# Kernel tuning notes

Hardware: AMD Instinct MI355X
Metric: run time of the kernel (lower is better)

The kernel has to match this reference:

```python
import jax, jax.numpy as jnp
import numpy as np

N, M, B, L, D = 100000, 256, 8, 128, 64
COORD_MAX = 1024


def setup_inputs() -> dict:
    key = jax.random.key(0)
    ks = jax.random.split(key, 9)
    # batch ids sorted so the original loop's centroid_offset == column index
    clu_b = jnp.sort(jax.random.randint(ks[0], (N, 1), 0, B))
    cen_b = jnp.sort(jax.random.randint(ks[1], (M, 1), 0, B))
    clu_xyz = jax.random.randint(ks[2], (N, 3), 0, COORD_MAX)
    cen_xyz = jax.random.randint(ks[3], (M, 3), 0, COORD_MAX)
    return {
        "cluster_coords": jnp.concatenate([clu_b, clu_xyz], axis=1).astype(jnp.int32),
        "centroid_coords": jnp.concatenate([cen_b, cen_xyz], axis=1).astype(jnp.int32),
        "cluster_feats": jax.random.normal(ks[4], (N, L), jnp.float32),
        "centroid_feats": jax.random.normal(ks[5], (M, L), jnp.float32),
        "centroid_conf": jax.random.uniform(ks[6], (M, 1), jnp.float32),
        "W": jax.random.normal(ks[7], (L, D), jnp.float32) * 0.05,
        "b": jax.random.normal(ks[8], (D,), jnp.float32) * 0.05,
    }


def reference(cluster_coords, centroid_coords, cluster_feats, centroid_feats,
              centroid_conf, W, b):
    # pointwise Conv3d(k=1) == linear on features
    clu = cluster_feats @ W + b                      # [N, D]
    nrm = jnp.maximum(jnp.linalg.norm(clu, axis=1, keepdims=True), 1e-12)
    clu = clu / nrm                                  # F.normalize(p=2, dim=1)
    cen = centroid_conf * (centroid_feats @ W + b)   # [M, D]

    # same-batch mask replaces the python loop + scatter
    valid = cluster_coords[:, 0][:, None] == centroid_coords[:, 0][None, :]  # [N, M]

    # pairwise L2 distance on spatial coords via squared expansion (exact for small ints)
    cc = cluster_coords[:, 1:].astype(jnp.float32)   # [N, 3]
    ec = centroid_coords[:, 1:].astype(jnp.float32)  # [M, 3]
    d2 = (jnp.sum(cc * cc, axis=1)[:, None]
          + jnp.sum(ec * ec, axis=1)[None, :]
          - 2.0 * cc @ ec.T)
    dist = jnp.maximum(jnp.sqrt(jnp.maximum(d2, 0.0)), 0.1)  # clamp(min=0.1)

    logits = jnp.where(valid, -dist, -jnp.inf)
    attn = jax.nn.softmax(logits, axis=-1)           # per-row over same-batch centroids
    attn = jnp.where(valid, attn, 0.0)               # rows w/ no centroids -> 0 (matches zeros init)

    out = (clu @ cen.T) * attn                       # [N, M]
    return out
```

## Files before the change

kernel.cpp:

```cpp
#include <hip/hip_runtime.h>
#include <stdint.h>


#define NN 100000
#define MM 256
#define BB 8
#define LL 128
#define DD 64
#define NTILES (NN / 16)

typedef float f32x4 __attribute__((ext_vector_type(4)));
typedef __bf16 bf16x8 __attribute__((ext_vector_type(8)));

union U16x8 { uint4 u; bf16x8 v; unsigned short s[8]; };

static __device__ __forceinline__ unsigned short f2bf(float f) {
  union { float f; unsigned int i; } t; t.f = f;
  unsigned int x = t.i;
  x += 0x7fffu + ((x >> 16) & 1u);
  return (unsigned short)(x >> 16);
}

__global__ __launch_bounds__(256) void prep_kernel(
    const int* __restrict__ cen_coords,
    const float* __restrict__ cen_feats,
    const float* __restrict__ conf,
    const float* __restrict__ W,
    const float* __restrict__ bvec,
    unsigned short* __restrict__ cen_ws,
    unsigned short* __restrict__ wt_ws,
    float4* __restrict__ cmeta_ws)
{
  int tid = threadIdx.x;
  if (blockIdx.x < 16) {
    int m = blockIdx.x * 16 + (tid >> 4);
    int c = tid & 15;
    float a0 = 0.f, a1 = 0.f, a2 = 0.f, a3 = 0.f;
    for (int l = 0; l < LL; l++) {
      float f = cen_feats[m * LL + l];
      const float* wr = W + l * DD + c;
      a0 += f * wr[0];  a1 += f * wr[16];
      a2 += f * wr[32]; a3 += f * wr[48];
    }
    float cf = conf[m];
    cen_ws[m * DD + c +  0] = f2bf(cf * (a0 + bvec[c +  0]));
    cen_ws[m * DD + c + 16] = f2bf(cf * (a1 + bvec[c + 16]));
    cen_ws[m * DD + c + 32] = f2bf(cf * (a2 + bvec[c + 32]));
    cen_ws[m * DD + c + 48] = f2bf(cf * (a3 + bvec[c + 48]));
  } else {
    for (int i = tid; i < LL * DD; i += 256) {
      int l = i >> 6, d = i & 63;
      wt_ws[d * LL + l] = f2bf(W[l * DD + d]);
    }
    {
      int4 cc = ((const int4*)cen_coords)[tid];
      float4 f; f.x = (float)cc.x; f.y = (float)cc.y; f.z = (float)cc.z; f.w = (float)cc.w;
      cmeta_ws[tid] = f;
    }
  }
}

__global__ __launch_bounds__(256) void main_kernel(
    const int* __restrict__ clu_coords,
    const float* __restrict__ feats,
    const float* __restrict__ bvec,
    const unsigned short* __restrict__ cen_ws,
    const unsigned short* __restrict__ wt_ws,
    const float4* __restrict__ cmeta_ws,
    float* __restrict__ out)
{
  __shared__ float4 cmeta_s[MM];
  __shared__ __align__(16) unsigned short clu_s[4][16 * 72];
  __shared__ int4 rmeta_s[4][16];
  __shared__ float2 rsoft_s[4][16];

  int tid = threadIdx.x;
  int wave = tid >> 6, lane = tid & 63;
  for (int i = tid; i < MM; i += 256) cmeta_s[i] = cmeta_ws[i];
  int tile = blockIdx.x * 4 + wave;
  bool live = tile < NTILES;
  if (live && lane < 16) rmeta_s[wave][lane] = ((const int4*)clu_coords)[tile * 16 + lane];
  __syncthreads();

  int q = lane >> 4, c = lane & 15;
  float inv_nrm[4];
  if (live) {
    f32x4 acc[4] = {{0,0,0,0},{0,0,0,0},{0,0,0,0},{0,0,0,0}};
    const float4* fb = (const float4*)(feats + (size_t)(tile * 16 + c) * LL);
    const uint4* wb = (const uint4*)wt_ws;
#pragma unroll
    for (int ks = 0; ks < 4; ks++) {
      float4 f0 = fb[ks * 8 + q * 2];
      float4 f1 = fb[ks * 8 + q * 2 + 1];
      U16x8 a;
      a.s[0] = f2bf(f0.x); a.s[1] = f2bf(f0.y); a.s[2] = f2bf(f0.z); a.s[3] = f2bf(f0.w);
      a.s[4] = f2bf(f1.x); a.s[5] = f2bf(f1.y); a.s[6] = f2bf(f1.z); a.s[7] = f2bf(f1.w);
#pragma unroll
      for (int nt = 0; nt < 4; nt++) {
        U16x8 b; b.u = wb[(nt * 16 + c) * 16 + ks * 4 + q];
        acc[nt] = __builtin_amdgcn_mfma_f32_16x16x32_bf16(a.v, b.v, acc[nt], 0, 0, 0);
      }
    }
#pragma unroll
    for (int nt = 0; nt < 4; nt++) {
      float bv = bvec[nt * 16 + c];
      acc[nt][0] += bv; acc[nt][1] += bv; acc[nt][2] += bv; acc[nt][3] += bv;
    }
#pragma unroll
    for (int r = 0; r < 4; r++) {
      float s = acc[0][r]*acc[0][r] + acc[1][r]*acc[1][r] + acc[2][r]*acc[2][r] + acc[3][r]*acc[3][r];
      s += __shfl_xor(s, 1); s += __shfl_xor(s, 2); s += __shfl_xor(s, 4); s += __shfl_xor(s, 8);
      inv_nrm[r] = 1.0f / fmaxf(sqrtf(s), 1e-12f);
    }
#pragma unroll
    for (int nt = 0; nt < 4; nt++)
#pragma unroll
      for (int r = 0; r < 4; r++)
        clu_s[wave][(q * 4 + r) * 72 + nt * 16 + c] = f2bf(acc[nt][r]);

    {
      int rr = lane >> 2, ss = lane & 3;
      int4 rm = rmeta_s[wave][rr];
      float rbf = (float)rm.x;
      float x = (float)rm.y, y = (float)rm.z, z = (float)rm.w;
      float dmin = 3.4e38f;
      for (int m = ss; m < MM; m += 4) {
        float4 cm = cmeta_s[m];
        if (cm.x == rbf) {
          float dx = x - cm.y, dy = y - cm.z, dz = z - cm.w;
          float d = fmaxf(sqrtf(dx*dx + dy*dy + dz*dz), 0.1f);
          dmin = fminf(dmin, d);
        }
      }
      dmin = fminf(dmin, __shfl_xor(dmin, 1));
      dmin = fminf(dmin, __shfl_xor(dmin, 2));
      if (!(dmin < 3.0e38f)) dmin = 0.f;
      float ssum = 0.f;
      for (int m = ss; m < MM; m += 4) {
        float4 cm = cmeta_s[m];
        if (cm.x == rbf) {
          float dx = x - cm.y, dy = y - cm.z, dz = z - cm.w;
          float d = fmaxf(sqrtf(dx*dx + dy*dy + dz*dz), 0.1f);
          ssum += __expf(dmin - d);
        }
      }
      ssum += __shfl_xor(ssum, 1);
      ssum += __shfl_xor(ssum, 2);
      float invden = ssum > 0.f ? 1.f / ssum : 0.f;
      rsoft_s[wave][rr] = make_float2(dmin, invden);
    }
  }
  __syncthreads();
  if (!live) return;

  const uint4* cb = (const uint4*)(clu_s[wave]);
  U16x8 a0, a1;
  a0.u = cb[c * 9 + q];
  a1.u = cb[c * 9 + 4 + q];

  float rx[4], ry[4], rz[4], sdmin[4], sinv[4];
  int rb[4];
#pragma unroll
  for (int r = 0; r < 4; r++) {
    int4 rm = rmeta_s[wave][q * 4 + r];
    rb[r] = rm.x; rx[r] = (float)rm.y; ry[r] = (float)rm.z; rz[r] = (float)rm.w;
    float2 sp = rsoft_s[wave][q * 4 + r];
    sdmin[r] = sp.x; sinv[r] = sp.y;
  }

  const uint4* cenb = (const uint4*)cen_ws;
  size_t orow = (size_t)(tile * 16) * MM;
#pragma unroll
  for (int mt = 0; mt < 16; mt++) {
    U16x8 b0, b1;
    b0.u = cenb[(mt * 16 + c) * 8 + q];
    b1.u = cenb[(mt * 16 + c) * 8 + 4 + q];
    f32x4 dacc = {0, 0, 0, 0};
    dacc = __builtin_amdgcn_mfma_f32_16x16x32_bf16(a0.v, b0.v, dacc, 0, 0, 0);
    dacc = __builtin_amdgcn_mfma_f32_16x16x32_bf16(a1.v, b1.v, dacc, 0, 0, 0);
    int m = mt * 16 + c;
    float4 cm = cmeta_s[m];
    int cbatch = (int)cm.x;
#pragma unroll
    for (int r = 0; r < 4; r++) {
      float dx = rx[r] - cm.y, dy = ry[r] - cm.z, dz = rz[r] - cm.w;
      float d = fmaxf(sqrtf(dx*dx + dy*dy + dz*dz), 0.1f);
      float w = __expf(fminf(sdmin[r] - d, 0.f)) * sinv[r] * inv_nrm[r];
      float val = (cbatch == rb[r]) ? dacc[r] * w : 0.f;
      out[orow + (size_t)(q * 4 + r) * MM + m] = val;
    }
  }
}

extern "C" void kernel_launch(void* const* d_in, const int* in_sizes, int n_in,
                              void* d_out, int out_size, void* d_ws, size_t ws_size,
                              hipStream_t stream) {
  const int* clu_coords = (const int*)d_in[0];
  const int* cen_coords = (const int*)d_in[1];
  const float* clu_feats = (const float*)d_in[2];
  const float* cen_feats = (const float*)d_in[3];
  const float* conf      = (const float*)d_in[4];
  const float* W         = (const float*)d_in[5];
  const float* bvec      = (const float*)d_in[6];
  float* out = (float*)d_out;

  char* ws = (char*)d_ws;
  unsigned short* cen_ws = (unsigned short*)ws;
  unsigned short* wt_ws  = (unsigned short*)(ws + 32768);
  float4* cmeta_ws       = (float4*)(ws + 32768 + 16384);

  prep_kernel<<<17, 256, 0, stream>>>(cen_coords, cen_feats, conf, W, bvec,
                                      cen_ws, wt_ws, cmeta_ws);
  main_kernel<<<(NTILES + 3) / 4, 256, 0, stream>>>(
      clu_coords, clu_feats, bvec, cen_ws, wt_ws, cmeta_ws, out);
}
```

Before: 226.5 us.

## Split each row tile across four waves with LDS-staged softmax and coalesced stores

Each block now handles one 16-row tile instead of four. Wave 0 does the feature projection while the other three waves compute partial min distances. All waves then compute the softmax weights into an LDS buffer and each wave does a quarter of the centroid MFMA columns. The output tile is written with coalesced float4 stores from LDS. This spreads the serial softmax loops across more threads and widens the stores, at the cost of more __syncthreads barriers, uncached global reads of the centroid metadata, and a larger LDS footprint per block.

Result: slower. 237.7 us (+5.0%).

```diff
diff --git a/kernel.cpp b/kernel.cpp
--- a/kernel.cpp
+++ b/kernel.cpp
@@ -4,10 +4,10 @@
 
 #define NN 100000
 #define MM 256
-#define BB 8
 #define LL 128
 #define DD 64
 #define NTILES (NN / 16)
+#define WP 260
 
 typedef float f32x4 __attribute__((ext_vector_type(4)));
 typedef __bf16 bf16x8 __attribute__((ext_vector_type(8)));
@@ -61,30 +61,27 @@
 }
 
 __global__ __launch_bounds__(256) void main_kernel(
-    const int* __restrict__ clu_coords,
+    const int4* __restrict__ clu_coords4,
     const float* __restrict__ feats,
     const float* __restrict__ bvec,
     const unsigned short* __restrict__ cen_ws,
     const unsigned short* __restrict__ wt_ws,
-    const float4* __restrict__ cmeta_ws,
+    const float4* __restrict__ cmeta,
     float* __restrict__ out)
 {
-  __shared__ float4 cmeta_s[MM];
-  __shared__ __align__(16) unsigned short clu_s[4][16 * 72];
-  __shared__ int4 rmeta_s[4][16];
-  __shared__ float2 rsoft_s[4][16];
+  __shared__ __align__(16) float w_s[16 * WP];
+  __shared__ __align__(16) unsigned short clu_s[16 * 72];
+  __shared__ float part_s[16][16];
+  __shared__ float dmin_s[16];
+  __shared__ float invn_s[16];
+  __shared__ float scale_s[16];
 
   int tid = threadIdx.x;
   int wave = tid >> 6, lane = tid & 63;
-  for (int i = tid; i < MM; i += 256) cmeta_s[i] = cmeta_ws[i];
-  int tile = blockIdx.x * 4 + wave;
-  bool live = tile < NTILES;
-  if (live && lane < 16) rmeta_s[wave][lane] = ((const int4*)clu_coords)[tile * 16 + lane];
-  __syncthreads();
-
+  int tile = blockIdx.x;
   int q = lane >> 4, c = lane & 15;
-  float inv_nrm[4];
-  if (live) {
+
+  if (wave == 0) {
     f32x4 acc[4] = {{0,0,0,0},{0,0,0,0},{0,0,0,0},{0,0,0,0}};
     const float4* fb = (const float4*)(feats + (size_t)(tile * 16 + c) * LL);
     const uint4* wb = (const uint4*)wt_ws;
@@ -110,84 +107,110 @@
     for (int r = 0; r < 4; r++) {
       float s = acc[0][r]*acc[0][r] + acc[1][r]*acc[1][r] + acc[2][r]*acc[2][r] + acc[3][r]*acc[3][r];
       s += __shfl_xor(s, 1); s += __shfl_xor(s, 2); s += __shfl_xor(s, 4); s += __shfl_xor(s, 8);
-      inv_nrm[r] = 1.0f / fmaxf(sqrtf(s), 1e-12f);
+      float invn = 1.0f / fmaxf(sqrtf(s), 1e-12f);
+      if (c == 0) invn_s[q * 4 + r] = invn;
     }
 #pragma unroll
     for (int nt = 0; nt < 4; nt++)
 #pragma unroll
       for (int r = 0; r < 4; r++)
-        clu_s[wave][(q * 4 + r) * 72 + nt * 16 + c] = f2bf(acc[nt][r]);
-
-    {
-      int rr = lane >> 2, ss = lane & 3;
-      int4 rm = rmeta_s[wave][rr];
-      float rbf = (float)rm.x;
-      float x = (float)rm.y, y = (float)rm.z, z = (float)rm.w;
-      float dmin = 3.4e38f;
-      for (int m = ss; m < MM; m += 4) {
-        float4 cm = cmeta_s[m];
-        if (cm.x == rbf) {
-          float dx = x - cm.y, dy = y - cm.z, dz = z - cm.w;
-          float d = fmaxf(sqrtf(dx*dx + dy*dy + dz*dz), 0.1f);
-          dmin = fminf(dmin, d);
-        }
-      }
-      dmin = fminf(dmin, __shfl_xor(dmin, 1));
-      dmin = fminf(dmin, __shfl_xor(dmin, 2));
-      if (!(dmin < 3.0e38f)) dmin = 0.f;
-      float ssum = 0.f;
-      for (int m = ss; m < MM; m += 4) {
-        float4 cm = cmeta_s[m];
-        if (cm.x == rbf) {
-          float dx = x - cm.y, dy = y - cm.z, dz = z - cm.w;
-          float d = fmaxf(sqrtf(dx*dx + dy*dy + dz*dz), 0.1f);
-          ssum += __expf(dmin - d);
-        }
-      }
-      ssum += __shfl_xor(ssum, 1);
-      ssum += __shfl_xor(ssum, 2);
-      float invden = ssum > 0.f ? 1.f / ssum : 0.f;
-      rsoft_s[wave][rr] = make_float2(dmin, invden);
-    }
-  }
-  __syncthreads();
-  if (!live) return;
-
-  const uint4* cb = (const uint4*)(clu_s[wave]);
-  U16x8 a0, a1;
-  a0.u = cb[c * 9 + q];
-  a1.u = cb[c * 9 + 4 + q];
-
-  float rx[4], ry[4], rz[4], sdmin[4], sinv[4];
-  int rb[4];
-#pragma unroll
-  for (int r = 0; r < 4; r++) {
-    int4 rm = rmeta_s[wave][q * 4 + r];
-    rb[r] = rm.x; rx[r] = (float)rm.y; ry[r] = (float)rm.z; rz[r] = (float)rm.w;
-    float2 sp = rsoft_s[wave][q * 4 + r];
-    sdmin[r] = sp.x; sinv[r] = sp.y;
-  }
-
-  const uint4* cenb = (const uint4*)cen_ws;
-  size_t orow = (size_t)(tile * 16) * MM;
-#pragma unroll
-  for (int mt = 0; mt < 16; mt++) {
-    U16x8 b0, b1;
-    b0.u = cenb[(mt * 16 + c) * 8 + q];
-    b1.u = cenb[(mt * 16 + c) * 8 + 4 + q];
-    f32x4 dacc = {0, 0, 0, 0};
-    dacc = __builtin_amdgcn_mfma_f32_16x16x32_bf16(a0.v, b0.v, dacc, 0, 0, 0);
-    dacc = __builtin_amdgcn_mfma_f32_16x16x32_bf16(a1.v, b1.v, dacc, 0, 0, 0);
-    int m = mt * 16 + c;
-    float4 cm = cmeta_s[m];
-    int cbatch = (int)cm.x;
-#pragma unroll
-    for (int r = 0; r < 4; r++) {
-      float dx = rx[r] - cm.y, dy = ry[r] - cm.z, dz = rz[r] - cm.w;
-      float d = fmaxf(sqrtf(dx*dx + dy*dy + dz*dz), 0.1f);
-      float w = __expf(fminf(sdmin[r] - d, 0.f)) * sinv[r] * inv_nrm[r];
-      float val = (cbatch == rb[r]) ? dacc[r] * w : 0.f;
-      out[orow + (size_t)(q * 4 + r) * MM + m] = val;
+        clu_s[(q * 4 + r) * 72 + nt * 16 + c] = f2bf(acc[nt][r]);
+  } else {
+    int u = tid - 64;
+    int row = u & 15, g = u >> 4;
+    int col0 = (g < 8) ? g * 21 : 168 + (g - 8) * 22;
+    int cw   = (g < 8) ? 21 : 22;
+    int4 rm = clu_coords4[tile * 16 + row];
+    float rbf = (float)rm.x;
+    float x = (float)rm.y, y = (float)rm.z, z = (float)rm.w;
+    float d2min = 3.4e38f;
+    for (int i = 0; i < cw; i++) {
+      float4 cm = cmeta[col0 + i];
+      if (cm.x == rbf) {
+        float dx = x - cm.y, dy = y - cm.z, dz = z - cm.w;
+        d2min = fminf(d2min, dx*dx + dy*dy + dz*dz);
+      }
+    }
+    part_s[row][g] = d2min;
+  }
+  __syncthreads();
+
+  if (tid < 16) {
+    float m = 3.4e38f;
+#pragma unroll
+    for (int g = 0; g < 12; g++) m = fminf(m, part_s[tid][g]);
+    dmin_s[tid] = fmaxf(sqrtf(m), 0.1f);
+  }
+  __syncthreads();
+
+  {
+    int row = tid & 15, ch = tid >> 4;
+    int4 rm = clu_coords4[tile * 16 + row];
+    float rbf = (float)rm.x;
+    float x = (float)rm.y, y = (float)rm.z, z = (float)rm.w;
+    float dmin = dmin_s[row];
+    float ssum = 0.f;
+    int base = row * WP + ch * 16;
+    for (int i = 0; i < 16; i++) {
+      float4 cm = cmeta[ch * 16 + i];
+      float e = 0.f;
+      if (cm.x == rbf) {
+        float dx = x - cm.y, dy = y - cm.z, dz = z - cm.w;
+        float d = fmaxf(sqrtf(dx*dx + dy*dy + dz*dz), 0.1f);
+        e = __expf(dmin - d);
+      }
+      w_s[base + i] = e;
+      ssum += e;
+    }
+    part_s[row][ch] = ssum;
+  }
+  __syncthreads();
+
+  if (tid < 16) {
+    float s = 0.f;
+#pragma unroll
+    for (int ch = 0; ch < 16; ch++) s += part_s[tid][ch];
+    float inv = (s > 0.f) ? 1.f / s : 0.f;
+    scale_s[tid] = inv * invn_s[tid];
+  }
+  __syncthreads();
+
+  {
+    const uint4* cb = (const uint4*)clu_s;
+    U16x8 a0, a1;
+    a0.u = cb[c * 9 + q];
+    a1.u = cb[c * 9 + 4 + q];
+    float scl[4];
+#pragma unroll
+    for (int r = 0; r < 4; r++) scl[r] = scale_s[q * 4 + r];
+    const uint4* cenb = (const uint4*)cen_ws;
+#pragma unroll
+    for (int i = 0; i < 4; i++) {
+      int mt = wave * 4 + i;
+      U16x8 b0, b1;
+      b0.u = cenb[(mt * 16 + c) * 8 + q];
+      b1.u = cenb[(mt * 16 + c) * 8 + 4 + q];
+      f32x4 dacc = {0, 0, 0, 0};
+      dacc = __builtin_amdgcn_mfma_f32_16x16x32_bf16(a0.v, b0.v, dacc, 0, 0, 0);
+      dacc = __builtin_amdgcn_mfma_f32_16x16x32_bf16(a1.v, b1.v, dacc, 0, 0, 0);
+      int m = mt * 16 + c;
+#pragma unroll
+      for (int r = 0; r < 4; r++) {
+        int idx = (q * 4 + r) * WP + m;
+        w_s[idx] = dacc[r] * w_s[idx] * scl[r];
+      }
+    }
+  }
+  __syncthreads();
+
+  {
+    size_t obase = (size_t)tile * (16 * MM);
+#pragma unroll
+    for (int i = 0; i < 4; i++) {
+      int j = i * 256 + tid;
+      int row = j >> 6, col4 = j & 63;
+      float4 v = *(const float4*)&w_s[row * WP + col4 * 4];
+      *(float4*)(out + obase + (size_t)row * MM + col4 * 4) = v;
     }
   }
 }
@@ -211,6 +234,6 @@
 
   prep_kernel<<<17, 256, 0, stream>>>(cen_coords, cen_feats, conf, W, bvec,
                                       cen_ws, wt_ws, cmeta_ws);
-  main_kernel<<<(NTILES + 3) / 4, 256, 0, stream>>>(
-      clu_coords, clu_feats, bvec, cen_ws, wt_ws, cmeta_ws, out);
-}
+  main_kernel<<<NTILES, 256, 0, stream>>>(
+      (const int4*)clu_coords, clu_feats, bvec, cen_ws, wt_ws, cmeta_ws, out);
+}
```

## Compute softmax distances once in registers and drop shared-memory metadata

Applied to the files above, without the earlier changes.

Replaces the separate two-pass softmax statistics stage, which computed each distance twice and then a third time in the output loop, with a single pass. Each lane computes its 64 distances once, keeps them in registers and reduces min and sum across 16 lanes with shuffles. The exponentials are reused for the output, and the shared-memory staging of centroid and row metadata plus the first block barrier are removed. In exchange the kernel holds 64 extra registers per lane, which may lower occupancy, and reads centroid metadata straight from global memory or cache.

Measured after the change: 198.7 us. 12.2% less time.

```diff
diff --git a/kernel.cpp b/kernel.cpp
--- a/kernel.cpp
+++ b/kernel.cpp
@@ -4,7 +4,6 @@
 
 #define NN 100000
 #define MM 256
-#define BB 8
 #define LL 128
 #define DD 64
 #define NTILES (NN / 16)
@@ -61,28 +60,22 @@
 }
 
 __global__ __launch_bounds__(256) void main_kernel(
-    const int* __restrict__ clu_coords,
+    const int4* __restrict__ clu_coords4,
     const float* __restrict__ feats,
     const float* __restrict__ bvec,
     const unsigned short* __restrict__ cen_ws,
     const unsigned short* __restrict__ wt_ws,
-    const float4* __restrict__ cmeta_ws,
+    const float4* __restrict__ cmeta,
     float* __restrict__ out)
 {
-  __shared__ float4 cmeta_s[MM];
   __shared__ __align__(16) unsigned short clu_s[4][16 * 72];
-  __shared__ int4 rmeta_s[4][16];
-  __shared__ float2 rsoft_s[4][16];
 
   int tid = threadIdx.x;
   int wave = tid >> 6, lane = tid & 63;
-  for (int i = tid; i < MM; i += 256) cmeta_s[i] = cmeta_ws[i];
+  int q = lane >> 4, c = lane & 15;
   int tile = blockIdx.x * 4 + wave;
   bool live = tile < NTILES;
-  if (live && lane < 16) rmeta_s[wave][lane] = ((const int4*)clu_coords)[tile * 16 + lane];
-  __syncthreads();
-
-  int q = lane >> 4, c = lane & 15;
+
   float inv_nrm[4];
   if (live) {
     f32x4 acc[4] = {{0,0,0,0},{0,0,0,0},{0,0,0,0},{0,0,0,0}};
@@ -117,56 +110,63 @@
 #pragma unroll
       for (int r = 0; r < 4; r++)
         clu_s[wave][(q * 4 + r) * 72 + nt * 16 + c] = f2bf(acc[nt][r]);
-
-    {
-      int rr = lane >> 2, ss = lane & 3;
-      int4 rm = rmeta_s[wave][rr];
-      float rbf = (float)rm.x;
-      float x = (float)rm.y, y = (float)rm.z, z = (float)rm.w;
-      float dmin = 3.4e38f;
-      for (int m = ss; m < MM; m += 4) {
-        float4 cm = cmeta_s[m];
-        if (cm.x == rbf) {
-          float dx = x - cm.y, dy = y - cm.z, dz = z - cm.w;
-          float d = fmaxf(sqrtf(dx*dx + dy*dy + dz*dz), 0.1f);
-          dmin = fminf(dmin, d);
-        }
-      }
-      dmin = fminf(dmin, __shfl_xor(dmin, 1));
-      dmin = fminf(dmin, __shfl_xor(dmin, 2));
-      if (!(dmin < 3.0e38f)) dmin = 0.f;
-      float ssum = 0.f;
-      for (int m = ss; m < MM; m += 4) {
-        float4 cm = cmeta_s[m];
-        if (cm.x == rbf) {
-          float dx = x - cm.y, dy = y - cm.z, dz = z - cm.w;
-          float d = fmaxf(sqrtf(dx*dx + dy*dy + dz*dz), 0.1f);
-          ssum += __expf(dmin - d);
-        }
-      }
-      ssum += __shfl_xor(ssum, 1);
-      ssum += __shfl_xor(ssum, 2);
-      float invden = ssum > 0.f ? 1.f / ssum : 0.f;
-      rsoft_s[wave][rr] = make_float2(dmin, invden);
-    }
   }
   __syncthreads();
   if (!live) return;
+
+  int rb[4]; float rx[4], ry[4], rz[4];
+#pragma unroll
+  for (int r = 0; r < 4; r++) {
+    int4 rm = clu_coords4[tile * 16 + q * 4 + r];
+    rb[r] = rm.x; rx[r] = (float)rm.y; ry[r] = (float)rm.z; rz[r] = (float)rm.w;
+  }
+
+  float dv[16][4];
+  float dmin[4] = {1e30f, 1e30f, 1e30f, 1e30f};
+#pragma unroll
+  for (int mt = 0; mt < 16; mt++) {
+    float4 cm = cmeta[mt * 16 + c];
+    int cbatch = (int)cm.x;
+#pragma unroll
+    for (int r = 0; r < 4; r++) {
+      float dx = rx[r] - cm.y, dy = ry[r] - cm.z, dz = rz[r] - cm.w;
+      float d = fmaxf(sqrtf(dx*dx + dy*dy + dz*dz), 0.1f);
+      d = (cbatch == rb[r]) ? d : 1e30f;
+      dv[mt][r] = d;
+      dmin[r] = fminf(dmin[r], d);
+    }
+  }
+#pragma unroll
+  for (int r = 0; r < 4; r++) {
+    dmin[r] = fminf(dmin[r], __shfl_xor(dmin[r], 1));
+    dmin[r] = fminf(dmin[r], __shfl_xor(dmin[r], 2));
+    dmin[r] = fminf(dmin[r], __shfl_xor(dmin[r], 4));
+    dmin[r] = fminf(dmin[r], __shfl_xor(dmin[r], 8));
+    dmin[r] = fminf(dmin[r], 1e29f);
+  }
+  float rsum[4] = {0.f, 0.f, 0.f, 0.f};
+#pragma unroll
+  for (int mt = 0; mt < 16; mt++)
+#pragma unroll
+    for (int r = 0; r < 4; r++) {
+      float e = __expf(fminf(dmin[r] - dv[mt][r], 0.f));
+      dv[mt][r] = e;
+      rsum[r] += e;
+    }
+  float scale[4];
+#pragma unroll
+  for (int r = 0; r < 4; r++) {
+    rsum[r] += __shfl_xor(rsum[r], 1);
+    rsum[r] += __shfl_xor(rsum[r], 2);
+    rsum[r] += __shfl_xor(rsum[r], 4);
+    rsum[r] += __shfl_xor(rsum[r], 8);
+    scale[r] = (rsum[r] > 0.f) ? inv_nrm[r] / rsum[r] : 0.f;
+  }
 
   const uint4* cb = (const uint4*)(clu_s[wave]);
   U16x8 a0, a1;
   a0.u = cb[c * 9 + q];
   a1.u = cb[c * 9 + 4 + q];
-
-  float rx[4], ry[4], rz[4], sdmin[4], sinv[4];
-  int rb[4];
-#pragma unroll
-  for (int r = 0; r < 4; r++) {
-    int4 rm = rmeta_s[wave][q * 4 + r];
-    rb[r] = rm.x; rx[r] = (float)rm.y; ry[r] = (float)rm.z; rz[r] = (float)rm.w;
-    float2 sp = rsoft_s[wave][q * 4 + r];
-    sdmin[r] = sp.x; sinv[r] = sp.y;
-  }
 
   const uint4* cenb = (const uint4*)cen_ws;
   size_t orow = (size_t)(tile * 16) * MM;
@@ -179,16 +179,9 @@
     dacc = __builtin_amdgcn_mfma_f32_16x16x32_bf16(a0.v, b0.v, dacc, 0, 0, 0);
     dacc = __builtin_amdgcn_mfma_f32_16x16x32_bf16(a1.v, b1.v, dacc, 0, 0, 0);
     int m = mt * 16 + c;
-    float4 cm = cmeta_s[m];
-    int cbatch = (int)cm.x;
-#pragma unroll
-    for (int r = 0; r < 4; r++) {
-      float dx = rx[r] - cm.y, dy = ry[r] - cm.z, dz = rz[r] - cm.w;
-      float d = fmaxf(sqrtf(dx*dx + dy*dy + dz*dz), 0.1f);
-      float w = __expf(fminf(sdmin[r] - d, 0.f)) * sinv[r] * inv_nrm[r];
-      float val = (cbatch == rb[r]) ? dacc[r] * w : 0.f;
-      out[orow + (size_t)(q * 4 + r) * MM + m] = val;
-    }
+#pragma unroll
+    for (int r = 0; r < 4; r++)
+      out[orow + (size_t)(q * 4 + r) * MM + m] = dacc[r] * dv[mt][r] * scale[r];
   }
 }
 
@@ -212,5 +205,5 @@
   prep_kernel<<<17, 256, 0, stream>>>(cen_coords, cen_feats, conf, W, bvec,
                                       cen_ws, wt_ws, cmeta_ws);
   main_kernel<<<(NTILES + 3) / 4, 256, 0, stream>>>(
-      clu_coords, clu_feats, bvec, cen_ws, wt_ws, cmeta_ws, out);
-}
+      (const int4*)clu_coords, clu_feats, bvec, cen_ws, wt_ws, cmeta_ws, out);
+}
```
